# Performance work log

Measured on AMD Instinct MI355X. Metric: run time of the kernel, lower is better.

Reference implementation:

```python
import jax, jax.numpy as jnp
import numpy as np

DIM = 768
NUM_HEADS = 12
HEAD_DIM = DIM // NUM_HEADS
SCALE = HEAD_DIM ** -0.5


def setup_inputs() -> dict:
    key = jax.random.key(0)
    ks = jax.random.split(key, 6)
    B, Lq, Lkv = 8, 1024, 1024
    return {
        "q": jax.random.normal(ks[0], (B, Lq, DIM), dtype=jnp.float32),
        "kv": jax.random.normal(ks[1], (B, Lkv, DIM), dtype=jnp.float32),
        "attn_pos": jax.random.normal(ks[2], (1, NUM_HEADS, Lq, Lkv), dtype=jnp.float32),
        "Wq": jax.random.normal(ks[3], (DIM, DIM), dtype=jnp.float32) * (DIM ** -0.5),
        "Wkv": jax.random.normal(ks[4], (2 * DIM, DIM), dtype=jnp.float32) * (DIM ** -0.5),
        "Wproj": jax.random.normal(ks[5], (DIM, DIM), dtype=jnp.float32) * (DIM ** -0.5),
        "bproj": jnp.zeros((DIM,), dtype=jnp.float32),
    }


def reference(q, kv, attn_pos, Wq, Wkv, Wproj, bproj):
    B, Lq, C = q.shape
    Lkv = kv.shape[1]
    H, D = NUM_HEADS, HEAD_DIM
    # q/kv projections (torch Linear: x @ W.T); attn_pos_encoding_only path
    qh = (q @ Wq.T).reshape(B, Lq, H, D).transpose(0, 2, 1, 3)        # (B,H,Lq,D)
    kvp = (kv @ Wkv.T).reshape(B, Lkv, 2, H, D).transpose(2, 0, 3, 1, 4)
    k, v = kvp[0], kvp[1]                                             # (B,H,Lkv,D)
    # scaled dot-product attention with additive positional bias
    attn = jnp.einsum('bhqd,bhkd->bhqk', qh, k) * SCALE + attn_pos    # (B,H,Lq,Lkv)
    attn = jax.nn.softmax(attn, axis=-1)
    x = jnp.einsum('bhqk,bhkd->bhqd', attn, v)                        # (B,H,Lq,D)
    x = x.transpose(0, 2, 1, 3).reshape(B, Lq, C)
    return x @ Wproj.T + bproj
```

## Files before the change

### kernel.cpp

```cpp
#include <hip/hip_runtime.h>

#define DIM 768
#define NHEADS 12
#define HDIM 64
#define BATCH 8
#define LQ 1024
#define LKV 1024
#define ATTN_SCALE 0.125f
#define LOG2E 1.4426950408889634f
#define EXP_SHIFT 14.426950408889634f

typedef __bf16 bf16;
typedef __bf16 bf16x4 __attribute__((ext_vector_type(4)));
typedef __bf16 bf16x8 __attribute__((ext_vector_type(8)));
typedef short s16x4 __attribute__((ext_vector_type(4)));
typedef float f32x4 __attribute__((ext_vector_type(4)));

union B4 { bf16x4 h; s16x4 s; };

static __device__ __forceinline__ f32x4 mfma_k32(bf16x8 a, bf16x8 b, f32x4 c) {
    return __builtin_amdgcn_mfma_f32_16x16x32_bf16(a, b, c, 0, 0, 0);
}
static __device__ __forceinline__ f32x4 mfma_k16(s16x4 a, s16x4 b, f32x4 c) {
    return __builtin_amdgcn_mfma_f32_16x16x16bf16_1k(a, b, c, 0, 0, 0);
}

static __device__ __forceinline__ void async16(const bf16* g, bf16* l) {
    __builtin_amdgcn_global_load_lds(
        (const __attribute__((address_space(1))) unsigned int*)g,
        (__attribute__((address_space(3))) unsigned int*)l, 16, 0, 0);
}
static __device__ __forceinline__ void drain_vmem() {
    __asm__ volatile("s_waitcnt vmcnt(0)" ::: "memory");
}

#define NQ4 (BATCH * LQ * DIM / 4)
#define NW4 (DIM * DIM / 4)
__global__ void cvt_all(const float4* __restrict__ q, const float4* __restrict__ kv,
                        const float4* __restrict__ Wq, const float4* __restrict__ Wkv,
                        const float4* __restrict__ Wp,
                        bf16x4* __restrict__ qb, bf16x4* __restrict__ kvb,
                        bf16x4* __restrict__ wall, bf16x4* __restrict__ wpb) {
    int i = blockIdx.x * 256 + threadIdx.x;
    const float4* src; bf16x4* dst; int j;
    if (i < NQ4)                { src = q;   dst = qb;        j = i; }
    else if (i < 2 * NQ4)       { src = kv;  dst = kvb;       j = i - NQ4; }
    else if (i < 2 * NQ4 + NW4) { src = Wq;  dst = wall;      j = i - 2 * NQ4; }
    else if (i < 2 * NQ4 + 3 * NW4) { src = Wkv; dst = wall + NW4; j = i - 2 * NQ4 - NW4; }
    else if (i < 2 * NQ4 + 4 * NW4) { src = Wp;  dst = wpb;   j = i - 2 * NQ4 - 3 * NW4; }
    else return;
    float4 v = src[j];
    bf16x4 o;
    o[0] = (bf16)v.x; o[1] = (bf16)v.y; o[2] = (bf16)v.z; o[3] = (bf16)v.w;
    dst[j] = o;
}

__global__ __launch_bounds__(256) void proj_gemm(
    const bf16* __restrict__ qb, const bf16* __restrict__ kvb,
    const bf16* __restrict__ W,
    bf16* __restrict__ Qp, bf16* __restrict__ Kp, bf16* __restrict__ Vt)
{
    __shared__ bf16 As[128 * 32];
    __shared__ bf16 Bs[128 * 32];
    const int tid  = threadIdx.x;
    const int lane = tid & 63;
    const int w    = tid >> 6;
    const int wm = (w >> 1) * 64;
    const int wn = (w & 1) * 64;
    const int m0 = blockIdx.x * 128;
    const int n0 = blockIdx.y * 128;
    const int K = DIM;
    const int lq = lane & 15;
    const int quad = lane >> 4;

    const bf16* A = (n0 < DIM) ? qb : kvb;
    const int isV = (n0 >= 2 * DIM);

    const int rl = lane >> 2;
    const int ck = (lane & 3) * 8;
    const bf16* gA = A + (size_t)(m0 + w * 32 + rl) * K + ck;
    const bf16* gB = W + (size_t)(n0 + w * 32 + rl) * K + ck;
    bf16* lA = &As[w * 1024];
    bf16* lB = &Bs[w * 1024];

    f32x4 acc[4][4] = {};

    for (int k0 = 0; k0 < K; k0 += 32) {
        async16(gA + k0,                  lA);
        async16(gA + (size_t)16 * K + k0, lA + 512);
        async16(gB + k0,                  lB);
        async16(gB + (size_t)16 * K + k0, lB + 512);
        drain_vmem();
        __syncthreads();

        bf16x8 a[4], b[4];
        #pragma unroll
        for (int i = 0; i < 4; i++)
            a[i] = *(const bf16x8*)&As[(wm + i * 16 + lq) * 32 + quad * 8];
        #pragma unroll
        for (int j = 0; j < 4; j++)
            b[j] = *(const bf16x8*)&Bs[(wn + j * 16 + lq) * 32 + quad * 8];
        if (isV) {
            #pragma unroll
            for (int i = 0; i < 4; i++)
                #pragma unroll
                for (int j = 0; j < 4; j++)
                    acc[i][j] = mfma_k32(a[i], b[j], acc[i][j]);
        } else {
            #pragma unroll
            for (int i = 0; i < 4; i++)
                #pragma unroll
                for (int j = 0; j < 4; j++)
                    acc[i][j] = mfma_k32(b[j], a[i], acc[i][j]);
        }
        __syncthreads();
    }

    if (isV) {
        const int n0v = n0 - 2 * DIM;
        #pragma unroll
        for (int i = 0; i < 4; i++) {
            const int base_m = m0 + wm + i * 16;
            const int b_idx = base_m >> 10;
            const int kvl = (base_m & 1023) + quad * 4;
            #pragma unroll
            for (int j = 0; j < 4; j++) {
                const int nl = n0v + wn + j * 16 + lq;
                const int h = nl >> 6;
                const int d = nl & 63;
                B4 pk;
                #pragma unroll
                for (int r = 0; r < 4; r++) pk.h[r] = (bf16)acc[i][j][r];
                *(s16x4*)&Vt[(((size_t)b_idx * NHEADS + h) * HDIM + d) * LKV + kvl] = pk.s;
            }
        }
    } else {
        bf16* Cb = (n0 < DIM) ? Qp : Kp;
        const int nb = (n0 < DIM) ? n0 : n0 - DIM;
        #pragma unroll
        for (int i = 0; i < 4; i++) {
            const size_t row = m0 + wm + i * 16 + lq;
            #pragma unroll
            for (int j = 0; j < 4; j++) {
                const int col = nb + wn + j * 16 + quad * 4;
                B4 pk;
                #pragma unroll
                for (int r = 0; r < 4; r++) pk.h[r] = (bf16)acc[i][j][r];
                *(s16x4*)&Cb[row * DIM + col] = pk.s;
            }
        }
    }
}

__global__ __launch_bounds__(256) void out_gemm(
    const bf16* __restrict__ A, const bf16* __restrict__ B,
    float* __restrict__ Cp, const float* __restrict__ bias, int M, int N, int K)
{
    __shared__ bf16 As[64 * 32];
    __shared__ bf16 Bs[128 * 32];
    const int tid  = threadIdx.x;
    const int lane = tid & 63;
    const int w    = tid >> 6;
    const int wm = (w >> 1) * 32;
    const int wn = (w & 1) * 64;
    const int m0 = blockIdx.x * 64;
    const int n0 = blockIdx.y * 128;
    const int lq = lane & 15;
    const int quad = lane >> 4;

    const int rl = lane >> 2;
    const int ck = (lane & 3) * 8;
    const bf16* gA = A + (size_t)(m0 + w * 16 + rl) * K + ck;
    const bf16* gB = B + (size_t)(n0 + w * 32 + rl) * K + ck;
    bf16* lA = &As[w * 512];
    bf16* lB = &Bs[w * 1024];

    f32x4 acc[2][4] = {};

    for (int k0 = 0; k0 < K; k0 += 32) {
        async16(gA + k0,                  lA);
        async16(gB + k0,                  lB);
        async16(gB + (size_t)16 * K + k0, lB + 512);
        drain_vmem();
        __syncthreads();

        bf16x8 a[2], b[4];
        #pragma unroll
        for (int i = 0; i < 2; i++)
            a[i] = *(const bf16x8*)&As[(wm + i * 16 + lq) * 32 + quad * 8];
        #pragma unroll
        for (int j = 0; j < 4; j++)
            b[j] = *(const bf16x8*)&Bs[(wn + j * 16 + lq) * 32 + quad * 8];
        #pragma unroll
        for (int i = 0; i < 2; i++)
            #pragma unroll
            for (int j = 0; j < 4; j++)
                acc[i][j] = mfma_k32(b[j], a[i], acc[i][j]);
        __syncthreads();
    }

    #pragma unroll
    for (int i = 0; i < 2; i++) {
        const size_t row = m0 + wm + i * 16 + lq;
        #pragma unroll
        for (int j = 0; j < 4; j++) {
            const int col = n0 + wn + j * 16 + quad * 4;
            float4 bj = *(const float4*)&bias[col];
            float4 o;
            o.x = acc[i][j][0] + bj.x; o.y = acc[i][j][1] + bj.y;
            o.z = acc[i][j][2] + bj.z; o.w = acc[i][j][3] + bj.w;
            *(float4*)&Cp[row * N + col] = o;
        }
    }
}

__global__ __launch_bounds__(256) void attn_kernel(
    const bf16* __restrict__ Qb,
    const bf16* __restrict__ Kb,
    const bf16* __restrict__ Vt,
    const float* __restrict__ pos,
    bf16* __restrict__ O)
{
    __shared__ bf16 Ks[64 * 72];
    __shared__ bf16 Vs[64 * 72];

    const int by = blockIdx.y;
    const int h = by >> 3, b = by & 7;
    const int bh = b * NHEADS + h;
    const int q0 = blockIdx.x * 64;
    const int t = threadIdx.x;
    const int lane = t & 63;
    const int w = t >> 6;
    const int lq = lane & 15;
    const int quad = lane >> 4;

    const bf16* qg = Qb + (size_t)(b * LQ + q0 + w * 16 + lq) * DIM + h * HDIM + quad * 8;
    bf16x8 qa[2];
    qa[0] = *(const bf16x8*)(qg);
    qa[1] = *(const bf16x8*)(qg + 32);

    float l_r = 0.f;
    f32x4 o_acc[4] = {};

    const float4* pos4 = (const float4*)(pos + ((size_t)h * LQ + q0 + w * 16 + lq) * LKV);

    for (int kv0 = 0; kv0 < LKV; kv0 += 64) {
        #pragma unroll
        for (int p = 0; p < 2; p++) {
            int row = (t >> 3) + p * 32;
            int c8  = (t & 7) * 8;
            *(uint4*)&Ks[row * 72 + c8] =
                *(const uint4*)(Kb + (size_t)(b * LKV + kv0 + row) * DIM + h * HDIM + c8);
            *(uint4*)&Vs[row * 72 + c8] =
                *(const uint4*)(Vt + (size_t)(bh * HDIM + row) * LKV + kv0 + c8);
        }
        __syncthreads();

        float4 pb[4];
        #pragma unroll
        for (int kvblk = 0; kvblk < 4; kvblk++)
            pb[kvblk] = pos4[(kv0 >> 2) + kvblk * 4 + quad];

        f32x4 sc[4];
        #pragma unroll
        for (int kvblk = 0; kvblk < 4; kvblk++) {
            sc[kvblk] = (f32x4){0.f, 0.f, 0.f, 0.f};
            #pragma unroll
            for (int kt = 0; kt < 2; kt++) {
                bf16x8 ak = *(const bf16x8*)&Ks[(kvblk * 16 + lq) * 72 + kt * 32 + quad * 8];
                sc[kvblk] = mfma_k32(ak, qa[kt], sc[kvblk]);
            }
        }

        B4 pfrag[4];
        #pragma unroll
        for (int kvblk = 0; kvblk < 4; kvblk++) {
            float pbv[4] = {pb[kvblk].x, pb[kvblk].y, pb[kvblk].z, pb[kvblk].w};
            #pragma unroll
            for (int r = 0; r < 4; r++) {
                float sv = fmaf(sc[kvblk][r], ATTN_SCALE, pbv[r]);
                float p = exp2f(fmaf(sv, LOG2E, -EXP_SHIFT));
                l_r += p;
                pfrag[kvblk].h[r] = (bf16)p;
            }
        }

        #pragma unroll
        for (int dblk = 0; dblk < 4; dblk++) {
            #pragma unroll
            for (int kvblk = 0; kvblk < 4; kvblk++) {
                s16x4 va = *(const s16x4*)&Vs[(dblk * 16 + lq) * 72 + kvblk * 16 + quad * 4];
                o_acc[dblk] = mfma_k16(va, pfrag[kvblk].s, o_acc[dblk]);
            }
        }
        __syncthreads();
    }

    l_r += __shfl_xor(l_r, 16);
    l_r += __shfl_xor(l_r, 32);
    float inv = 1.f / l_r;
    const size_t orow = (size_t)(b * LQ + q0 + w * 16 + lq) * DIM + h * HDIM;
    #pragma unroll
    for (int dblk = 0; dblk < 4; dblk++) {
        B4 ob;
        #pragma unroll
        for (int r = 0; r < 4; r++) ob.h[r] = (bf16)(o_acc[dblk][r] * inv);
        *(s16x4*)&O[orow + dblk * 16 + quad * 4] = ob.s;
    }
}

extern "C" void kernel_launch(void* const* d_in, const int* in_sizes, int n_in,
                              void* d_out, int out_size, void* d_ws, size_t ws_size,
                              hipStream_t stream) {
    const float* q     = (const float*)d_in[0];
    const float* kv    = (const float*)d_in[1];
    const float* pos   = (const float*)d_in[2];
    const float* Wq    = (const float*)d_in[3];
    const float* Wkv   = (const float*)d_in[4];
    const float* Wproj = (const float*)d_in[5];
    const float* bproj = (const float*)d_in[6];
    float* out = (float*)d_out;

    char* ws = (char*)d_ws;
    size_t off = 0;
    auto alloc = [&](size_t bytes) -> void* {
        void* p = ws + off;
        off += (bytes + 255) & ~(size_t)255;
        return p;
    };

    const int M = BATCH * LQ;
    bf16* qb   = (bf16*)alloc((size_t)M * DIM * 2);
    bf16* kvb  = (bf16*)alloc((size_t)M * DIM * 2);
    bf16* wall = (bf16*)alloc((size_t)3 * DIM * DIM * 2);
    bf16* wpb  = (bf16*)alloc((size_t)DIM * DIM * 2);
    bf16* Qp   = (bf16*)alloc((size_t)M * DIM * 2);
    bf16* Kp   = (bf16*)alloc((size_t)M * DIM * 2);
    bf16* Vt   = (bf16*)alloc((size_t)BATCH * NHEADS * HDIM * LKV * 2);
    bf16* Ob   = (bf16*)alloc((size_t)M * DIM * 2);

    {
        int total = 2 * NQ4 + 4 * NW4;
        cvt_all<<<(total + 255) / 256, 256, 0, stream>>>(
            (const float4*)q, (const float4*)kv, (const float4*)Wq,
            (const float4*)Wkv, (const float4*)Wproj,
            (bf16x4*)qb, (bf16x4*)kvb, (bf16x4*)wall, (bf16x4*)wpb);
    }

    proj_gemm<<<dim3(M / 128, (3 * DIM) / 128), 256, 0, stream>>>(qb, kvb, wall, Qp, Kp, Vt);
    attn_kernel<<<dim3(LQ / 64, NHEADS * BATCH), 256, 0, stream>>>(Qp, Kp, Vt, pos, Ob);
    out_gemm<<<dim3(M / 64, DIM / 128), 256, 0, stream>>>(Ob, wpb, out, bproj, M, DIM, DIM);
}
```

Measured before the change: 297.6 us.

## Double-buffer GEMM and attention tiles, precompute fp16 log2-scaled position bias

Adds two-stage LDS double buffering to the projection and output GEMMs so the next K-slice loads while MFMAs run. The attention kernel prefetches K, V and bias into registers for the next tile and commits them to a second LDS buffer after compute. A new kernel converts the positional bias to fp16 pre-multiplied by log2e, reusing the qb workspace, which halves bias bytes read by attention and folds the scale into one FMA. The constant exp shift is dropped, and fp16 bias adds precision loss and an extra conversion pass.

```diff
diff --git a/kernel.cpp b/kernel.cpp
--- a/kernel.cpp
+++ b/kernel.cpp
@@ -8,13 +8,15 @@
 #define LKV 1024
 #define ATTN_SCALE 0.125f
 #define LOG2E 1.4426950408889634f
-#define EXP_SHIFT 14.426950408889634f
+#define C1_SL2E 0.18033688011112042f
 
 typedef __bf16 bf16;
 typedef __bf16 bf16x4 __attribute__((ext_vector_type(4)));
 typedef __bf16 bf16x8 __attribute__((ext_vector_type(8)));
 typedef short s16x4 __attribute__((ext_vector_type(4)));
 typedef float f32x4 __attribute__((ext_vector_type(4)));
+typedef _Float16 f16;
+typedef f16 f16x4 __attribute__((ext_vector_type(4)));
 
 union B4 { bf16x4 h; s16x4 s; };
 
@@ -36,6 +38,7 @@
 
 #define NQ4 (BATCH * LQ * DIM / 4)
 #define NW4 (DIM * DIM / 4)
+#define NP4 (NHEADS * LQ * LKV / 4)
 __global__ void cvt_all(const float4* __restrict__ q, const float4* __restrict__ kv,
                         const float4* __restrict__ Wq, const float4* __restrict__ Wkv,
                         const float4* __restrict__ Wp,
@@ -55,13 +58,23 @@
     dst[j] = o;
 }
 
+__global__ void cvt_pos(const float4* __restrict__ pos, f16x4* __restrict__ posh) {
+    int i = blockIdx.x * 256 + threadIdx.x;
+    if (i >= NP4) return;
+    float4 v = pos[i];
+    f16x4 o;
+    o[0] = (f16)(v.x * LOG2E); o[1] = (f16)(v.y * LOG2E);
+    o[2] = (f16)(v.z * LOG2E); o[3] = (f16)(v.w * LOG2E);
+    posh[i] = o;
+}
+
 __global__ __launch_bounds__(256) void proj_gemm(
     const bf16* __restrict__ qb, const bf16* __restrict__ kvb,
     const bf16* __restrict__ W,
     bf16* __restrict__ Qp, bf16* __restrict__ Kp, bf16* __restrict__ Vt)
 {
-    __shared__ bf16 As[128 * 32];
-    __shared__ bf16 Bs[128 * 32];
+    __shared__ bf16 As[2][128 * 32];
+    __shared__ bf16 Bs[2][128 * 32];
     const int tid  = threadIdx.x;
     const int lane = tid & 63;
     const int w    = tid >> 6;
@@ -80,26 +93,34 @@
     const int ck = (lane & 3) * 8;
     const bf16* gA = A + (size_t)(m0 + w * 32 + rl) * K + ck;
     const bf16* gB = W + (size_t)(n0 + w * 32 + rl) * K + ck;
-    bf16* lA = &As[w * 1024];
-    bf16* lB = &Bs[w * 1024];
 
     f32x4 acc[4][4] = {};
 
-    for (int k0 = 0; k0 < K; k0 += 32) {
+    auto stage = [&](int k0, int bufi) {
+        bf16* lA = &As[bufi][w * 1024];
+        bf16* lB = &Bs[bufi][w * 1024];
         async16(gA + k0,                  lA);
         async16(gA + (size_t)16 * K + k0, lA + 512);
         async16(gB + k0,                  lB);
         async16(gB + (size_t)16 * K + k0, lB + 512);
-        drain_vmem();
-        __syncthreads();
+    };
+
+    stage(0, 0);
+    drain_vmem();
+    __syncthreads();
+
+    for (int k0 = 0; k0 < K; k0 += 32) {
+        const int cur = (k0 >> 5) & 1;
+        const bool more = (k0 + 32 < K);
+        if (more) stage(k0 + 32, cur ^ 1);
 
         bf16x8 a[4], b[4];
         #pragma unroll
         for (int i = 0; i < 4; i++)
-            a[i] = *(const bf16x8*)&As[(wm + i * 16 + lq) * 32 + quad * 8];
+            a[i] = *(const bf16x8*)&As[cur][(wm + i * 16 + lq) * 32 + quad * 8];
         #pragma unroll
         for (int j = 0; j < 4; j++)
-            b[j] = *(const bf16x8*)&Bs[(wn + j * 16 + lq) * 32 + quad * 8];
+            b[j] = *(const bf16x8*)&Bs[cur][(wn + j * 16 + lq) * 32 + quad * 8];
         if (isV) {
             #pragma unroll
             for (int i = 0; i < 4; i++)
@@ -113,6 +134,8 @@
                 for (int j = 0; j < 4; j++)
                     acc[i][j] = mfma_k32(b[j], a[i], acc[i][j]);
         }
+
+        if (more) drain_vmem();
         __syncthreads();
     }
 
@@ -156,8 +179,8 @@
     const bf16* __restrict__ A, const bf16* __restrict__ B,
     float* __restrict__ Cp, const float* __restrict__ bias, int M, int N, int K)
 {
-    __shared__ bf16 As[64 * 32];
-    __shared__ bf16 Bs[128 * 32];
+    __shared__ bf16 As[2][64 * 32];
+    __shared__ bf16 Bs[2][128 * 32];
     const int tid  = threadIdx.x;
     const int lane = tid & 63;
     const int w    = tid >> 6;
@@ -172,30 +195,40 @@
     const int ck = (lane & 3) * 8;
     const bf16* gA = A + (size_t)(m0 + w * 16 + rl) * K + ck;
     const bf16* gB = B + (size_t)(n0 + w * 32 + rl) * K + ck;
-    bf16* lA = &As[w * 512];
-    bf16* lB = &Bs[w * 1024];
 
     f32x4 acc[2][4] = {};
 
-    for (int k0 = 0; k0 < K; k0 += 32) {
+    auto stage = [&](int k0, int bufi) {
+        bf16* lA = &As[bufi][w * 512];
+        bf16* lB = &Bs[bufi][w * 1024];
         async16(gA + k0,                  lA);
         async16(gB + k0,                  lB);
         async16(gB + (size_t)16 * K + k0, lB + 512);
-        drain_vmem();
-        __syncthreads();
+    };
+
+    stage(0, 0);
+    drain_vmem();
+    __syncthreads();
+
+    for (int k0 = 0; k0 < K; k0 += 32) {
+        const int cur = (k0 >> 5) & 1;
+        const bool more = (k0 + 32 < K);
+        if (more) stage(k0 + 32, cur ^ 1);
 
         bf16x8 a[2], b[4];
         #pragma unroll
         for (int i = 0; i < 2; i++)
-            a[i] = *(const bf16x8*)&As[(wm + i * 16 + lq) * 32 + quad * 8];
+            a[i] = *(const bf16x8*)&As[cur][(wm + i * 16 + lq) * 32 + quad * 8];
         #pragma unroll
         for (int j = 0; j < 4; j++)
-            b[j] = *(const bf16x8*)&Bs[(wn + j * 16 + lq) * 32 + quad * 8];
+            b[j] = *(const bf16x8*)&Bs[cur][(wn + j * 16 + lq) * 32 + quad * 8];
         #pragma unroll
         for (int i = 0; i < 2; i++)
             #pragma unroll
             for (int j = 0; j < 4; j++)
                 acc[i][j] = mfma_k32(b[j], a[i], acc[i][j]);
+
+        if (more) drain_vmem();
         __syncthreads();
     }
 
@@ -218,11 +251,11 @@
     const bf16* __restrict__ Qb,
     const bf16* __restrict__ Kb,
     const bf16* __restrict__ Vt,
-    const float* __restrict__ pos,
+    const f16*  __restrict__ posh,
     bf16* __restrict__ O)
 {
-    __shared__ bf16 Ks[64 * 72];
-    __shared__ bf16 Vs[64 * 72];
+    __shared__ bf16 Ks[2][64 * 72];
+    __shared__ bf16 Vs[2][64 * 72];
 
     const int by = blockIdx.y;
     const int h = by >> 3, b = by & 7;
@@ -239,27 +272,46 @@
     qa[0] = *(const bf16x8*)(qg);
     qa[1] = *(const bf16x8*)(qg + 32);
 
+    const int srow = t >> 3;
+    const int sc8  = (t & 7) * 8;
+    const bf16* Kg = Kb + (size_t)(b * LKV + srow) * DIM + h * HDIM + sc8;
+    const bf16* Vg = Vt + (size_t)(bh * HDIM + srow) * LKV + sc8;
+    const f16*  pg = posh + ((size_t)h * LQ + q0 + w * 16 + lq) * LKV + quad * 4;
+
+    uint4 kreg[2], vreg[2];
+    f16x4 preg[4];
+
+    auto stage = [&](int kv0) {
+        #pragma unroll
+        for (int p = 0; p < 2; p++) {
+            kreg[p] = *(const uint4*)(Kg + (size_t)(kv0 + p * 32) * DIM);
+            vreg[p] = *(const uint4*)(Vg + (size_t)(p * 32) * LKV + kv0);
+        }
+        #pragma unroll
+        for (int kb = 0; kb < 4; kb++)
+            preg[kb] = *(const f16x4*)(pg + kv0 + kb * 16);
+    };
+    auto commit = [&](int bufi) {
+        #pragma unroll
+        for (int p = 0; p < 2; p++) {
+            *(uint4*)&Ks[bufi][(srow + p * 32) * 72 + sc8] = kreg[p];
+            *(uint4*)&Vs[bufi][(srow + p * 32) * 72 + sc8] = vreg[p];
+        }
+    };
+
     float l_r = 0.f;
     f32x4 o_acc[4] = {};
 
-    const float4* pos4 = (const float4*)(pos + ((size_t)h * LQ + q0 + w * 16 + lq) * LKV);
-
-    for (int kv0 = 0; kv0 < LKV; kv0 += 64) {
-        #pragma unroll
-        for (int p = 0; p < 2; p++) {
-            int row = (t >> 3) + p * 32;
-            int c8  = (t & 7) * 8;
-            *(uint4*)&Ks[row * 72 + c8] =
-                *(const uint4*)(Kb + (size_t)(b * LKV + kv0 + row) * DIM + h * HDIM + c8);
-            *(uint4*)&Vs[row * 72 + c8] =
-                *(const uint4*)(Vt + (size_t)(bh * HDIM + row) * LKV + kv0 + c8);
-        }
-        __syncthreads();
-
-        float4 pb[4];
-        #pragma unroll
-        for (int kvblk = 0; kvblk < 4; kvblk++)
-            pb[kvblk] = pos4[(kv0 >> 2) + kvblk * 4 + quad];
+    stage(0);
+    commit(0);
+    __syncthreads();
+
+    for (int it = 0; it < LKV / 64; it++) {
+        const int cur = it & 1;
+        f16x4 pcur[4];
+        #pragma unroll
+        for (int kb = 0; kb < 4; kb++) pcur[kb] = preg[kb];
+        if (it + 1 < LKV / 64) stage((it + 1) * 64);
 
         f32x4 sc[4];
         #pragma unroll
@@ -267,7 +319,7 @@
             sc[kvblk] = (f32x4){0.f, 0.f, 0.f, 0.f};
             #pragma unroll
             for (int kt = 0; kt < 2; kt++) {
-                bf16x8 ak = *(const bf16x8*)&Ks[(kvblk * 16 + lq) * 72 + kt * 32 + quad * 8];
+                bf16x8 ak = *(const bf16x8*)&Ks[cur][(kvblk * 16 + lq) * 72 + kt * 32 + quad * 8];
                 sc[kvblk] = mfma_k32(ak, qa[kt], sc[kvblk]);
             }
         }
@@ -275,11 +327,9 @@
         B4 pfrag[4];
         #pragma unroll
         for (int kvblk = 0; kvblk < 4; kvblk++) {
-            float pbv[4] = {pb[kvblk].x, pb[kvblk].y, pb[kvblk].z, pb[kvblk].w};
             #pragma unroll
             for (int r = 0; r < 4; r++) {
-                float sv = fmaf(sc[kvblk][r], ATTN_SCALE, pbv[r]);
-                float p = exp2f(fmaf(sv, LOG2E, -EXP_SHIFT));
+                float p = exp2f(fmaf(sc[kvblk][r], C1_SL2E, (float)pcur[kvblk][r]));
                 l_r += p;
                 pfrag[kvblk].h[r] = (bf16)p;
             }
@@ -289,10 +339,12 @@
         for (int dblk = 0; dblk < 4; dblk++) {
             #pragma unroll
             for (int kvblk = 0; kvblk < 4; kvblk++) {
-                s16x4 va = *(const s16x4*)&Vs[(dblk * 16 + lq) * 72 + kvblk * 16 + quad * 4];
+                s16x4 va = *(const s16x4*)&Vs[cur][(dblk * 16 + lq) * 72 + kvblk * 16 + quad * 4];
                 o_acc[dblk] = mfma_k16(va, pfrag[kvblk].s, o_acc[dblk]);
             }
         }
+
+        if (it + 1 < LKV / 64) commit(cur ^ 1);
         __syncthreads();
     }
 
@@ -338,6 +390,7 @@
     bf16* Kp   = (bf16*)alloc((size_t)M * DIM * 2);
     bf16* Vt   = (bf16*)alloc((size_t)BATCH * NHEADS * HDIM * LKV * 2);
     bf16* Ob   = (bf16*)alloc((size_t)M * DIM * 2);
+    f16* posh  = (f16*)qb;
 
     {
         int total = 2 * NQ4 + 4 * NW4;
@@ -348,6 +401,7 @@
     }
 
     proj_gemm<<<dim3(M / 128, (3 * DIM) / 128), 256, 0, stream>>>(qb, kvb, wall, Qp, Kp, Vt);
-    attn_kernel<<<dim3(LQ / 64, NHEADS * BATCH), 256, 0, stream>>>(Qp, Kp, Vt, pos, Ob);
+    cvt_pos<<<NP4 / 256, 256, 0, stream>>>((const float4*)pos, (f16x4*)posh);
+    attn_kernel<<<dim3(LQ / 64, NHEADS * BATCH), 256, 0, stream>>>(Qp, Kp, Vt, posh, Ob);
     out_gemm<<<dim3(M / 64, DIM / 128), 256, 0, stream>>>(Ob, wpb, out, bproj, M, DIM, DIM);
 }
```

New measurement: 387.1 us. +30.1%, slower.
